# Optimization experiments

Hardware: AMD Instinct MI355X
Metric: run time of the kernel (lower is better)

Reference implementation:

```python
import jax, jax.numpy as jnp
import numpy as np

B, S, H, HS, BLK = 4, 4096, 16, 1024, 64
D = HS // H


def setup_inputs() -> dict:
    key = jax.random.key(0)
    ks = jax.random.split(key, 7)
    s = np.float32(1.0 / np.sqrt(HS))
    return {
        "hidden_states": jax.random.normal(ks[0], (B, S, HS), jnp.float32),
        "Wq": jax.random.normal(ks[1], (HS, HS), jnp.float32) * s,
        "bq": jax.random.normal(ks[2], (HS,), jnp.float32) * s,
        "Wk": jax.random.normal(ks[3], (HS, HS), jnp.float32) * s,
        "bk": jax.random.normal(ks[4], (HS,), jnp.float32) * s,
        "Wv": jax.random.normal(ks[5], (HS, HS), jnp.float32) * s,
        "bv": jax.random.normal(ks[6], (HS,), jnp.float32) * s,
    }


def reference(hidden_states, Wq, bq, Wk, bk, Wv, bv):
    b, m, _ = hidden_states.shape
    h, d, wm = H, D, BLK
    wn = wm
    nb = m // wm  # number of blocks
    scale = np.float32(1.0 / np.sqrt(d))

    def heads(x):  # [b, m, hs] -> [b, h, m, d]
        return x.reshape(b, m, h, d).transpose(0, 2, 1, 3)

    q = heads(hidden_states @ Wq.T + bq)
    k = heads(hidden_states @ Wk.T + bk)
    v = heads(hidden_states @ Wv.T + bv)

    qb = q.reshape(b, h, nb, wm, d)
    kb = k.reshape(b, h, nb, wn, d)
    vb = v.reshape(b, h, nb, wn, d)

    def attend(qx, kx, vx):  # qx [b,h,Q,d], kx/vx [b,h,K,d]
        scores = jnp.einsum('bhqd,bhkd->bhqk', qx, kx) * scale
        return jnp.einsum('bhqk,bhkd->bhqd', jax.nn.softmax(scores, axis=-1), vx)

    # first block: full attention over all keys
    first_ctx = attend(qb[:, :, 0], k, v)[:, :, None]

    # second block: keys = blocks [0, 1, 2, -1]
    k2 = jnp.concatenate([kb[:, :, 0], kb[:, :, 1], kb[:, :, 2], kb[:, :, -1]], axis=2)
    v2 = jnp.concatenate([vb[:, :, 0], vb[:, :, 1], vb[:, :, 2], vb[:, :, -1]], axis=2)
    second_ctx = attend(qb[:, :, 1], k2, v2)[:, :, None]

    # middle blocks 2..nb-3: sliding window of 3 key blocks + global first/last
    exp_k = jnp.concatenate([kb[:, :, 1:-3], kb[:, :, 2:-2], kb[:, :, 3:-1]], axis=3)  # [b,h,l,3wn,d]
    exp_v = jnp.concatenate([vb[:, :, 1:-3], vb[:, :, 2:-2], vb[:, :, 3:-1]], axis=3)
    mq = qb[:, :, 2:-2]  # [b,h,l,wm,d]
    inner = jnp.einsum('bhlqd,bhlkd->bhlqk', mq, exp_k) * scale
    first_band = jnp.einsum('bhlqd,bhkd->bhlqk', mq, kb[:, :, 0]) * scale
    last_band = jnp.einsum('bhlqd,bhkd->bhlqk', mq, kb[:, :, -1]) * scale
    band = jnp.concatenate([first_band, inner, last_band], axis=-1)  # [b,h,l,wm,5wn]
    aw = jax.nn.softmax(band, axis=-1)
    mid_ctx = jnp.einsum('bhlqk,bhlkd->bhlqd', aw[..., wn:4 * wn], exp_v)
    mid_ctx = mid_ctx + jnp.einsum('bhlqk,bhkd->bhlqd', aw[..., :wn], vb[:, :, 0])
    mid_ctx = mid_ctx + jnp.einsum('bhlqk,bhkd->bhlqd', aw[..., -wn:], vb[:, :, -1])

    # second-to-last block: keys = blocks [0, -3, -2, -1]
    k3 = jnp.concatenate([kb[:, :, 0], kb[:, :, -3], kb[:, :, -2], kb[:, :, -1]], axis=2)
    v3 = jnp.concatenate([vb[:, :, 0], vb[:, :, -3], vb[:, :, -2], vb[:, :, -1]], axis=2)
    second_last_ctx = attend(qb[:, :, -2], k3, v3)[:, :, None]

    # last block: full attention over all keys
    last_ctx = attend(qb[:, :, -1], k, v)[:, :, None]

    ctx = jnp.concatenate([first_ctx, second_ctx, mid_ctx, second_last_ctx, last_ctx], axis=2)
    return ctx.reshape(b, h, m, d).transpose(0, 2, 1, 3).reshape(b, m, h * d)
```

## Files before the change

kernel.cpp:

```cpp
#include <hip/hip_runtime.h>

typedef unsigned short u16;
using f32x4  = __attribute__((ext_vector_type(4))) float;
using bf16x8 = __attribute__((ext_vector_type(8))) short;

#define SEQ 4096
#define HS  1024
#define NHEAD 16
#define DH  64

__device__ __forceinline__ u16 f2bf(float f) {
  unsigned u = __float_as_uint(f);
  unsigned r = (u + 0x7fffu + ((u >> 16) & 1u)) >> 16;
  return (u16)r;
}

__device__ __forceinline__ void gl_lds16(const void* g, void* l) {
  __builtin_amdgcn_global_load_lds(
      (const __attribute__((address_space(1))) unsigned int*)g,
      (__attribute__((address_space(3))) unsigned int*)l, 16, 0, 0);
}

#define LGKM0 asm volatile("s_waitcnt lgkmcnt(0)" ::: "memory")
#define BARR  __builtin_amdgcn_s_barrier()

__global__ void cvt_all(const float* __restrict__ X, const float* __restrict__ Wq,
                        const float* __restrict__ Wk, const float* __restrict__ Wv,
                        u16* __restrict__ dst) {
  const int N = 19922944;
  int idx = blockIdx.x * blockDim.x + threadIdx.x;
  int stride = gridDim.x * blockDim.x;
  for (int i = idx * 4; i < N; i += stride * 4) {
    const float* s;
    if (i < 16777216)       s = X  + i;
    else if (i < 17825792)  s = Wq + (i - 16777216);
    else if (i < 18874368)  s = Wk + (i - 17825792);
    else                    s = Wv + (i - 18874368);
    float4 v = *reinterpret_cast<const float4*>(s);
    u16 o0 = f2bf(v.x), o1 = f2bf(v.y), o2 = f2bf(v.z), o3 = f2bf(v.w);
    unsigned lo = (unsigned)o0 | ((unsigned)o1 << 16);
    unsigned hi = (unsigned)o2 | ((unsigned)o3 << 16);
    uint2 pk; pk.x = lo; pk.y = hi;
    *reinterpret_cast<uint2*>(dst + i) = pk;
  }
}

__global__ __launch_bounds__(512) void gemm_qkv8(
    const u16* __restrict__ X,
    const u16* __restrict__ Wq, const u16* __restrict__ Wk, const u16* __restrict__ Wv,
    const float* __restrict__ bq, const float* __restrict__ bk, const float* __restrict__ bv,
    u16* __restrict__ Q, u16* __restrict__ K, u16* __restrict__ V) {
  __shared__ u16 lds[65536];

  const int tid = threadIdx.x;
  const int l = tid & 63;
  const int w = tid >> 6;
  const int wr = w >> 2;
  const int wc = w & 3;
  const int c = l & 15;
  const int g = l >> 4;

  int i = blockIdx.x;
  int k8 = i & 7, j8 = i >> 3;
  int w2 = j8 >> 5, r8 = j8 & 31;
  int np = w2 * 4 + (r8 >> 3);
  int mp = k8 * 8 + (r8 & 7);
  const int m0 = mp * 256;
  const int mat = np >> 2;
  const int n0 = (np & 3) * 256;
  const u16* W = (mat == 0) ? Wq : (mat == 1) ? Wk : Wv;
  const float* bias = (mat == 0) ? bq : (mat == 1) ? bk : bv;
  u16* O = (mat == 0) ? Q : (mat == 1) ? K : V;

  f32x4 acc[2][4][4] = {};

  auto stage = [&](const u16* G, int gbase, int ktile, int kh, int which) {
    u16* region = lds + ((ktile & 1) * 32768 + which * 16384 + kh * 8192);
#pragma unroll
    for (int ii = 0; ii < 2; ++ii) {
      int chunk = w * 2 + ii;
      int srow = chunk * 8 + (l >> 3);
      int slot = (l & 7) ^ (l >> 3);
      int grow = srow + ((slot >> 2) << 7);
      int ke = ktile * 64 + kh * 32 + (slot & 3) * 8;
      gl_lds16(G + (size_t)(gbase + grow) * HS + ke, region + chunk * 512);
    }
  };

  auto readA = [&](int cur, int CH, int KH, bf16x8* aq) {
    const char* base = (const char*)lds + cur * 65536 + KH * 16384;
    int colb = (wr * 64 + g * 16) ^ ((c & 7) << 4);
#pragma unroll
    for (int mf = 0; mf < 4; ++mf)
      aq[mf] = *reinterpret_cast<const bf16x8*>(base + (CH * 64 + mf * 16 + c) * 128 + colb);
  };
  auto readB = [&](int cur, int KH, bf16x8* bq2) {
    const char* base = (const char*)lds + cur * 65536 + 32768 + KH * 16384;
    int colb = ((wc >> 1) * 64 + g * 16) ^ ((c & 7) << 4);
#pragma unroll
    for (int nf = 0; nf < 4; ++nf)
      bq2[nf] = *reinterpret_cast<const bf16x8*>(base + ((wc & 1) * 64 + nf * 16 + c) * 128 + colb);
  };
  auto mma16 = [&](bf16x8* aq, bf16x8* bq2, f32x4 (*accr)[4]) {
    __builtin_amdgcn_s_setprio(1);
#pragma unroll
    for (int mf = 0; mf < 4; ++mf)
#pragma unroll
      for (int nf = 0; nf < 4; ++nf)
        accr[mf][nf] = __builtin_amdgcn_mfma_f32_16x16x32_bf16(aq[mf], bq2[nf], accr[mf][nf], 0, 0, 0);
    __builtin_amdgcn_s_setprio(0);
  };

  stage(X, m0, 0, 0, 0); stage(W, n0, 0, 0, 1);
  stage(X, m0, 0, 1, 0); stage(W, n0, 0, 1, 1);
  stage(X, m0, 1, 0, 0); stage(W, n0, 1, 0, 1);
  asm volatile("s_waitcnt vmcnt(4)" ::: "memory");
  BARR;

  for (int j = 0; j < 16; ++j) {
    const int cur = j & 1;
    bf16x8 aq[4], bq2[4];
    readA(cur, 0, 0, aq); readB(cur, 0, bq2);
    if (j + 1 < 16) stage(X, m0, j + 1, 1, 0);
    BARR; LGKM0; mma16(aq, bq2, acc[0]); BARR;
    readA(cur, 1, 0, aq);
    if (j + 1 < 16) stage(W, n0, j + 1, 1, 1);
    BARR; LGKM0; mma16(aq, bq2, acc[1]); BARR;
    readA(cur, 0, 1, aq); readB(cur, 1, bq2);
    if (j + 2 < 16) stage(X, m0, j + 2, 0, 0);
    BARR; LGKM0; mma16(aq, bq2, acc[0]); BARR;
    readA(cur, 1, 1, aq);
    if (j + 2 < 16) stage(W, n0, j + 2, 0, 1);
    BARR; LGKM0; mma16(aq, bq2, acc[1]);
    if (j < 14)       asm volatile("s_waitcnt vmcnt(4)" ::: "memory");
    else if (j == 14) asm volatile("s_waitcnt vmcnt(0)" ::: "memory");
    BARR;
  }

  __syncthreads();
  {
    u16* cst = lds;
#pragma unroll 1
    for (int p = 0; p < 2; ++p) {
      if (wr == p) {
#pragma unroll
        for (int nf = 0; nf < 4; ++nf) {
          int cc = wc * 64 + nf * 16 + c;
          float bval = bias[n0 + cc];
#pragma unroll
          for (int ch = 0; ch < 2; ++ch)
#pragma unroll
            for (int mf = 0; mf < 4; ++mf)
#pragma unroll
              for (int jj = 0; jj < 4; ++jj) {
                int rl = ch * 64 + mf * 16 + g * 4 + jj;
                cst[rl * 260 + cc] = f2bf(acc[ch][mf][nf][jj] + bval);
              }
        }
      }
      __syncthreads();
#pragma unroll
      for (int i2 = 0; i2 < 8; ++i2) {
        int row = i2 * 16 + (tid >> 5);
        int colu = (tid & 31) * 8;
        bf16x8 vv = *reinterpret_cast<const bf16x8*>(cst + row * 260 + colu);
        *reinterpret_cast<bf16x8*>(O + (size_t)(m0 + p * 128 + row) * HS + n0 + colu) = vv;
      }
      __syncthreads();
    }
  }
}

__global__ void bigbird_attn2(const u16* __restrict__ Q, const u16* __restrict__ K,
                              const u16* __restrict__ V, float* __restrict__ OUT,
                              float* __restrict__ Opart, float* __restrict__ MLpart) {
  __shared__ u16 Qs[64 * 64];
  __shared__ u16 Ks[2][64 * 64];
  __shared__ u16 Vt[64 * 72];
  __shared__ u16 Ps[64 * 72];

  const int tid = threadIdx.x;
  const int lane = tid & 63;
  const int w = tid >> 6;
  const int g = lane >> 4;
  const int c = lane & 15;

  int bid = blockIdx.x;
  int L = (bid & 7) * 624 + (bid >> 3);
  int g_bh = L / 78;
  int r = L - g_bh * 78;
  int b = g_bh & 3, h = g_bh >> 2;

  int qb, nkb, seg8 = 0, p = 0;
  bool heavy;
  if (r < 62) {
    heavy = false;
    qb = r + 1;
    nkb = (qb == 1 || qb == 62) ? 4 : 5;
  } else {
    heavy = true;
    int s = r - 62;
    int q2 = s >> 3, seg = s & 7;
    qb = q2 ? 63 : 0; seg8 = seg * 8; nkb = 8;
    p = ((q2 * 16 + h) * 4 + b) * 8 + seg;
  }

  const size_t base_bh = (size_t)b * SEQ * HS + (size_t)h * DH;

  auto kb_of = [&](int it) -> int {
    if (heavy) return seg8 + it;
    if (qb == 1)  return (it == 3) ? 63 : it;
    if (qb == 62) return (it == 0) ? 0 : 60 + it;
    return (it == 0) ? 0 : ((it == 4) ? 63 : qb - 2 + it);
  };

  const int vkrow = tid & 63;
  const int vdseg = (tid >> 6) * 16;

  {
    const u16* qg = Q + base_bh + (size_t)qb * 64 * HS;
#pragma unroll
    for (int t2 = 0; t2 < 2; ++t2) {
      int sub = w * 2 + t2;
      int rr = sub * 8 + (lane >> 3);
      int c16 = (lane & 7) ^ (rr & 7);
      gl_lds16(qg + (size_t)rr * HS + c16 * 8, Qs + sub * 512);
    }
  }
  int kb0 = kb_of(0);
  {
    const u16* kg = K + base_bh + (size_t)kb0 * 64 * HS;
#pragma unroll
    for (int t2 = 0; t2 < 2; ++t2) {
      int sub = w * 2 + t2;
      int rr = sub * 8 + (lane >> 3);
      int c16 = (lane & 7) ^ (rr & 7);
      gl_lds16(kg + (size_t)rr * HS + c16 * 8, Ks[0] + sub * 512);
    }
  }
  bf16x8 vr0, vr1;
  {
    const u16* vg = V + base_bh + (size_t)kb0 * 64 * HS;
    vr0 = *reinterpret_cast<const bf16x8*>(vg + (size_t)vkrow * HS + vdseg);
    vr1 = *reinterpret_cast<const bf16x8*>(vg + (size_t)vkrow * HS + vdseg + 8);
  }
  __syncthreads();

  bf16x8 qf[2];
#pragma unroll
  for (int ks = 0; ks < 2; ++ks) {
    int rr = w * 16 + c;
    int c16 = (ks * 4 + g) ^ (rr & 7);
    qf[ks] = *reinterpret_cast<const bf16x8*>(Qs + rr * 64 + c16 * 8);
  }

  float m_run = -1e30f, l_run = 0.f;
  f32x4 o_acc[4] = {};
  const float scale = 0.125f;

  for (int it = 0; it < nkb; ++it) {
    const int cur = it & 1;
    {
#pragma unroll
      for (int j2 = 0; j2 < 8; ++j2) {
        Vt[(vdseg + j2) * 72 + vkrow]     = (u16)vr0[j2];
        Vt[(vdseg + 8 + j2) * 72 + vkrow] = (u16)vr1[j2];
      }
    }
    if (it + 1 < nkb) {
      int kbn = kb_of(it + 1);
      const u16* kg = K + base_bh + (size_t)kbn * 64 * HS;
#pragma unroll
      for (int t2 = 0; t2 < 2; ++t2) {
        int sub = w * 2 + t2;
        int rr = sub * 8 + (lane >> 3);
        int c16 = (lane & 7) ^ (rr & 7);
        gl_lds16(kg + (size_t)rr * HS + c16 * 8, Ks[cur ^ 1] + sub * 512);
      }
      const u16* vg = V + base_bh + (size_t)kbn * 64 * HS;
      vr0 = *reinterpret_cast<const bf16x8*>(vg + (size_t)vkrow * HS + vdseg);
      vr1 = *reinterpret_cast<const bf16x8*>(vg + (size_t)vkrow * HS + vdseg + 8);
    }

    f32x4 accs[4] = {};
#pragma unroll
    for (int ks = 0; ks < 2; ++ks) {
#pragma unroll
      for (int mf = 0; mf < 4; ++mf) {
        int rr = mf * 16 + c;
        int c16 = (ks * 4 + g) ^ (rr & 7);
        bf16x8 kf = *reinterpret_cast<const bf16x8*>(Ks[cur] + rr * 64 + c16 * 8);
        accs[mf] = __builtin_amdgcn_mfma_f32_16x16x32_bf16(kf, qf[ks], accs[mf], 0, 0, 0);
      }
    }

    float sv[16];
    float smax = -1e30f;
#pragma unroll
    for (int mf = 0; mf < 4; ++mf)
#pragma unroll
      for (int j = 0; j < 4; ++j) {
        float s = accs[mf][j] * scale;
        sv[mf * 4 + j] = s;
        smax = fmaxf(smax, s);
      }
    smax = fmaxf(smax, __shfl_xor(smax, 16));
    smax = fmaxf(smax, __shfl_xor(smax, 32));
    float m_new = fmaxf(m_run, smax);
    float corr = __expf(m_run - m_new);
    float psum = 0.f;
    u16 pb[16];
#pragma unroll
    for (int i = 0; i < 16; ++i) {
      float pv = __expf(sv[i] - m_new);
      psum += pv;
      pb[i] = f2bf(pv);
    }
    psum += __shfl_xor(psum, 16);
    psum += __shfl_xor(psum, 32);
    l_run = l_run * corr + psum;
    m_run = m_new;

#pragma unroll
    for (int j = 0; j < 4; ++j) {
      float cj = __shfl(corr, g * 4 + j);
#pragma unroll
      for (int df = 0; df < 4; ++df) o_acc[df][j] *= cj;
    }

    {
      int rr = w * 16 + c;
#pragma unroll
      for (int mf = 0; mf < 4; ++mf) {
        unsigned lo = (unsigned)pb[mf * 4 + 0] | ((unsigned)pb[mf * 4 + 1] << 16);
        unsigned hi = (unsigned)pb[mf * 4 + 2] | ((unsigned)pb[mf * 4 + 3] << 16);
        uint2 pk; pk.x = lo; pk.y = hi;
        *reinterpret_cast<uint2*>(Ps + rr * 72 + mf * 16 + g * 4) = pk;
      }
    }

    __syncthreads();

#pragma unroll
    for (int ks = 0; ks < 2; ++ks) {
      bf16x8 pf = *reinterpret_cast<const bf16x8*>(Ps + (w * 16 + c) * 72 + ks * 32 + g * 8);
#pragma unroll
      for (int df = 0; df < 4; ++df) {
        bf16x8 vf = *reinterpret_cast<const bf16x8*>(Vt + (df * 16 + c) * 72 + ks * 32 + g * 8);
        o_acc[df] = __builtin_amdgcn_mfma_f32_16x16x32_bf16(pf, vf, o_acc[df], 0, 0, 0);
      }
    }

    __syncthreads();
  }

  if (!heavy) {
#pragma unroll
    for (int j = 0; j < 4; ++j) {
      float lr = __shfl(l_run, g * 4 + j);
      float inv = 1.f / lr;
      int rr = qb * 64 + w * 16 + g * 4 + j;
      size_t rowbase = ((size_t)b * SEQ + rr) * HS + (size_t)h * DH;
#pragma unroll
      for (int df = 0; df < 4; ++df)
        OUT[rowbase + df * 16 + c] = o_acc[df][j] * inv;
    }
  } else {
#pragma unroll
    for (int j = 0; j < 4; ++j) {
      int row = w * 16 + g * 4 + j;
#pragma unroll
      for (int df = 0; df < 4; ++df)
        Opart[(size_t)p * 4096 + row * 64 + df * 16 + c] = o_acc[df][j];
    }
    if (g == 0) {
      int row = w * 16 + c;
      MLpart[(size_t)p * 128 + row * 2]     = m_run;
      MLpart[(size_t)p * 128 + row * 2 + 1] = l_run;
    }
  }
}

__global__ void bigbird_combine(const float* __restrict__ Opart, const float* __restrict__ MLpart,
                                float* __restrict__ OUT) {
  int bid = blockIdx.x >> 2;
  int quarter = blockIdx.x & 3;
  int b = bid & 3; int t = bid >> 2; int h = t & 15; int q2 = t >> 4;
  int qb = q2 ? 63 : 0;
  int w = threadIdx.x >> 6, lane = threadIdx.x & 63;
  int pbase = ((q2 * 16 + h) * 4 + b) * 8;
#pragma unroll 1
  for (int j2 = 0; j2 < 4; ++j2) {
    int rr = quarter * 4 + j2;
    int row = w * 16 + rr;
    float ms[8], ls[8];
    float M = -1e30f;
#pragma unroll
    for (int s = 0; s < 8; ++s) {
      ms[s] = MLpart[(size_t)(pbase + s) * 128 + row * 2];
      ls[s] = MLpart[(size_t)(pbase + s) * 128 + row * 2 + 1];
      M = fmaxf(M, ms[s]);
    }
    float L = 0.f, acc = 0.f;
#pragma unroll
    for (int s = 0; s < 8; ++s) {
      float e = __expf(ms[s] - M);
      L += ls[s] * e;
      acc += e * Opart[(size_t)(pbase + s) * 4096 + row * 64 + lane];
    }
    int rq = qb * 64 + row;
    OUT[((size_t)b * SEQ + rq) * HS + (size_t)h * DH + lane] = acc / L;
  }
}

extern "C" void kernel_launch(void* const* d_in, const int* in_sizes, int n_in,
                              void* d_out, int out_size, void* d_ws, size_t ws_size,
                              hipStream_t stream) {
  const float* X  = (const float*)d_in[0];
  const float* Wq = (const float*)d_in[1];
  const float* bq = (const float*)d_in[2];
  const float* Wk = (const float*)d_in[3];
  const float* bk = (const float*)d_in[4];
  const float* Wv = (const float*)d_in[5];
  const float* bv = (const float*)d_in[6];
  float* out = (float*)d_out;

  u16* Xb  = (u16*)d_ws;
  u16* Wqb = Xb + 16777216;
  u16* Wkb = Wqb + 1048576;
  u16* Wvb = Wkb + 1048576;
  u16* Qb  = Wvb + 1048576;
  u16* Kb  = Qb + 16777216;
  u16* Vb  = Kb + 16777216;

  float* Opart  = (float*)Xb;
  float* MLpart = (float*)Wqb;

  cvt_all<<<2048, 256, 0, stream>>>(X, Wq, Wk, Wv, Xb);
  gemm_qkv8<<<768, 512, 0, stream>>>(Xb, Wqb, Wkb, Wvb, bq, bk, bv, Qb, Kb, Vb);
  bigbird_attn2<<<4992, 256, 0, stream>>>(Qb, Kb, Vb, out, Opart, MLpart);
  bigbird_combine<<<512, 256, 0, stream>>>(Opart, MLpart, out);
}
```

Measured before the change: 224.8 us.

## Pair adjacent query blocks per workgroup to share K/V tile loads

The attention kernel now handles two query blocks per 512-thread workgroup. It iterates over the union of their key blocks (6 for adjacent middle blocks) and masks out the key block that does not belong to each query half. This roughly halves K/V global loads and LDS staging per query block, and pairs the two heavy global rows with each other. In exchange, each workgroup does extra masked QK/softmax/PV work (6 iterations for two blocks versus 5 each) and runs half as many workgroups.

```diff
diff --git a/kernel.cpp b/kernel.cpp
--- a/kernel.cpp
+++ b/kernel.cpp
@@ -171,87 +171,78 @@
   }
 }
 
-__global__ void bigbird_attn2(const u16* __restrict__ Q, const u16* __restrict__ K,
-                              const u16* __restrict__ V, float* __restrict__ OUT,
-                              float* __restrict__ Opart, float* __restrict__ MLpart) {
-  __shared__ u16 Qs[64 * 64];
+__global__ __launch_bounds__(512) void bigbird_attn3(
+    const u16* __restrict__ Q, const u16* __restrict__ K,
+    const u16* __restrict__ V, float* __restrict__ OUT,
+    float* __restrict__ Opart, float* __restrict__ MLpart) {
+  __shared__ u16 Qs[2][64 * 64];
   __shared__ u16 Ks[2][64 * 64];
   __shared__ u16 Vt[64 * 72];
-  __shared__ u16 Ps[64 * 72];
+  __shared__ u16 Ps[128 * 72];
 
   const int tid = threadIdx.x;
   const int lane = tid & 63;
   const int w = tid >> 6;
+  const int w4 = w & 3;
+  const int qsel = w >> 2;
   const int g = lane >> 4;
   const int c = lane & 15;
 
   int bid = blockIdx.x;
-  int L = (bid & 7) * 624 + (bid >> 3);
-  int g_bh = L / 78;
-  int r = L - g_bh * 78;
+  int L = (bid & 7) * 312 + (bid >> 3);
+  int g_bh = L / 39;
+  int r = L - g_bh * 39;
   int b = g_bh & 3, h = g_bh >> 2;
 
-  int qb, nkb, seg8 = 0, p = 0;
-  bool heavy;
-  if (r < 62) {
-    heavy = false;
-    qb = r + 1;
-    nkb = (qb == 1 || qb == 62) ? 4 : 5;
-  } else {
-    heavy = true;
-    int s = r - 62;
-    int q2 = s >> 3, seg = s & 7;
-    qb = q2 ? 63 : 0; seg8 = seg * 8; nkb = 8;
-    p = ((q2 * 16 + h) * 4 + b) * 8 + seg;
-  }
+  int qbA, qbB, nkb, seg = 0;
+  bool heavy = false;
+  if (r < 30)       { qbA = 2 + 2 * r; qbB = qbA + 1; nkb = 6; }
+  else if (r == 30) { qbA = 1; qbB = 62; nkb = 6; }
+  else              { heavy = true; qbA = 0; qbB = 63; seg = r - 31; nkb = 8; }
 
   const size_t base_bh = (size_t)b * SEQ * HS + (size_t)h * DH;
+  const int myqb = qsel ? qbB : qbA;
 
   auto kb_of = [&](int it) -> int {
-    if (heavy) return seg8 + it;
-    if (qb == 1)  return (it == 3) ? 63 : it;
-    if (qb == 62) return (it == 0) ? 0 : 60 + it;
-    return (it == 0) ? 0 : ((it == 4) ? 63 : qb - 2 + it);
-  };
-
-  const int vkrow = tid & 63;
-  const int vdseg = (tid >> 6) * 16;
-
-  {
-    const u16* qg = Q + base_bh + (size_t)qb * 64 * HS;
-#pragma unroll
-    for (int t2 = 0; t2 < 2; ++t2) {
-      int sub = w * 2 + t2;
-      int rr = sub * 8 + (lane >> 3);
-      int c16 = (lane & 7) ^ (rr & 7);
-      gl_lds16(qg + (size_t)rr * HS + c16 * 8, Qs + sub * 512);
-    }
+    if (heavy) return seg * 8 + it;
+    if (r == 30) return (it < 3) ? it : 58 + it;
+    return (it == 0) ? 0 : ((it == 5) ? 63 : (qbA - 2 + it));
+  };
+  auto masked_of = [&](int it) -> bool {
+    if (heavy) return false;
+    if (r == 30) return qsel ? (it == 1 || it == 2) : (it == 3 || it == 4);
+    return qsel ? (it == 1) : (it == 4);
+  };
+
+#pragma unroll
+  for (int t2 = 0; t2 < 2; ++t2) {
+    const u16* qg = Q + base_bh + (size_t)(t2 ? qbB : qbA) * 64 * HS;
+    int rr = w * 8 + (lane >> 3);
+    int c16 = (lane & 7) ^ (rr & 7);
+    gl_lds16(qg + (size_t)rr * HS + c16 * 8, Qs[t2] + w * 512);
   }
   int kb0 = kb_of(0);
   {
     const u16* kg = K + base_bh + (size_t)kb0 * 64 * HS;
-#pragma unroll
-    for (int t2 = 0; t2 < 2; ++t2) {
-      int sub = w * 2 + t2;
-      int rr = sub * 8 + (lane >> 3);
-      int c16 = (lane & 7) ^ (rr & 7);
-      gl_lds16(kg + (size_t)rr * HS + c16 * 8, Ks[0] + sub * 512);
-    }
-  }
-  bf16x8 vr0, vr1;
+    int rr = w * 8 + (lane >> 3);
+    int c16 = (lane & 7) ^ (rr & 7);
+    gl_lds16(kg + (size_t)rr * HS + c16 * 8, Ks[0] + w * 512);
+  }
+  const int vkrow = lane;
+  const int vd8 = w * 8;
+  bf16x8 vr;
   {
     const u16* vg = V + base_bh + (size_t)kb0 * 64 * HS;
-    vr0 = *reinterpret_cast<const bf16x8*>(vg + (size_t)vkrow * HS + vdseg);
-    vr1 = *reinterpret_cast<const bf16x8*>(vg + (size_t)vkrow * HS + vdseg + 8);
+    vr = *reinterpret_cast<const bf16x8*>(vg + (size_t)vkrow * HS + vd8);
   }
   __syncthreads();
 
   bf16x8 qf[2];
 #pragma unroll
   for (int ks = 0; ks < 2; ++ks) {
-    int rr = w * 16 + c;
+    int rr = w4 * 16 + c;
     int c16 = (ks * 4 + g) ^ (rr & 7);
-    qf[ks] = *reinterpret_cast<const bf16x8*>(Qs + rr * 64 + c16 * 8);
+    qf[ks] = *reinterpret_cast<const bf16x8*>(Qs[qsel] + rr * 64 + c16 * 8);
   }
 
   float m_run = -1e30f, l_run = 0.f;
@@ -260,31 +251,22 @@
 
   for (int it = 0; it < nkb; ++it) {
     const int cur = it & 1;
-    {
-#pragma unroll
-      for (int j2 = 0; j2 < 8; ++j2) {
-        Vt[(vdseg + j2) * 72 + vkrow]     = (u16)vr0[j2];
-        Vt[(vdseg + 8 + j2) * 72 + vkrow] = (u16)vr1[j2];
-      }
-    }
+#pragma unroll
+    for (int j2 = 0; j2 < 8; ++j2)
+      Vt[(vd8 + j2) * 72 + vkrow] = (u16)vr[j2];
     if (it + 1 < nkb) {
       int kbn = kb_of(it + 1);
       const u16* kg = K + base_bh + (size_t)kbn * 64 * HS;
-#pragma unroll
-      for (int t2 = 0; t2 < 2; ++t2) {
-        int sub = w * 2 + t2;
-        int rr = sub * 8 + (lane >> 3);
-        int c16 = (lane & 7) ^ (rr & 7);
-        gl_lds16(kg + (size_t)rr * HS + c16 * 8, Ks[cur ^ 1] + sub * 512);
-      }
+      int rr = w * 8 + (lane >> 3);
+      int c16 = (lane & 7) ^ (rr & 7);
+      gl_lds16(kg + (size_t)rr * HS + c16 * 8, Ks[cur ^ 1] + w * 512);
       const u16* vg = V + base_bh + (size_t)kbn * 64 * HS;
-      vr0 = *reinterpret_cast<const bf16x8*>(vg + (size_t)vkrow * HS + vdseg);
-      vr1 = *reinterpret_cast<const bf16x8*>(vg + (size_t)vkrow * HS + vdseg + 8);
+      vr = *reinterpret_cast<const bf16x8*>(vg + (size_t)vkrow * HS + vd8);
     }
 
     f32x4 accs[4] = {};
 #pragma unroll
-    for (int ks = 0; ks < 2; ++ks) {
+    for (int ks = 0; ks < 2; ++ks)
 #pragma unroll
       for (int mf = 0; mf < 4; ++mf) {
         int rr = mf * 16 + c;
@@ -292,15 +274,15 @@
         bf16x8 kf = *reinterpret_cast<const bf16x8*>(Ks[cur] + rr * 64 + c16 * 8);
         accs[mf] = __builtin_amdgcn_mfma_f32_16x16x32_bf16(kf, qf[ks], accs[mf], 0, 0, 0);
       }
-    }
-
+
+    const bool msk = masked_of(it);
     float sv[16];
     float smax = -1e30f;
 #pragma unroll
     for (int mf = 0; mf < 4; ++mf)
 #pragma unroll
       for (int j = 0; j < 4; ++j) {
-        float s = accs[mf][j] * scale;
+        float s = msk ? -1e30f : accs[mf][j] * scale;
         sv[mf * 4 + j] = s;
         smax = fmaxf(smax, s);
       }
@@ -329,7 +311,7 @@
     }
 
     {
-      int rr = w * 16 + c;
+      int rr = qsel * 64 + w4 * 16 + c;
 #pragma unroll
       for (int mf = 0; mf < 4; ++mf) {
         unsigned lo = (unsigned)pb[mf * 4 + 0] | ((unsigned)pb[mf * 4 + 1] << 16);
@@ -343,7 +325,8 @@
 
 #pragma unroll
     for (int ks = 0; ks < 2; ++ks) {
-      bf16x8 pf = *reinterpret_cast<const bf16x8*>(Ps + (w * 16 + c) * 72 + ks * 32 + g * 8);
+      bf16x8 pf = *reinterpret_cast<const bf16x8*>(
+          Ps + (qsel * 64 + w4 * 16 + c) * 72 + ks * 32 + g * 8);
 #pragma unroll
       for (int df = 0; df < 4; ++df) {
         bf16x8 vf = *reinterpret_cast<const bf16x8*>(Vt + (df * 16 + c) * 72 + ks * 32 + g * 8);
@@ -359,22 +342,23 @@
     for (int j = 0; j < 4; ++j) {
       float lr = __shfl(l_run, g * 4 + j);
       float inv = 1.f / lr;
-      int rr = qb * 64 + w * 16 + g * 4 + j;
+      int rr = myqb * 64 + w4 * 16 + g * 4 + j;
       size_t rowbase = ((size_t)b * SEQ + rr) * HS + (size_t)h * DH;
 #pragma unroll
       for (int df = 0; df < 4; ++df)
         OUT[rowbase + df * 16 + c] = o_acc[df][j] * inv;
     }
   } else {
+    int p = ((qsel * 16 + h) * 4 + b) * 8 + seg;
 #pragma unroll
     for (int j = 0; j < 4; ++j) {
-      int row = w * 16 + g * 4 + j;
+      int row = w4 * 16 + g * 4 + j;
 #pragma unroll
       for (int df = 0; df < 4; ++df)
         Opart[(size_t)p * 4096 + row * 64 + df * 16 + c] = o_acc[df][j];
     }
     if (g == 0) {
-      int row = w * 16 + c;
+      int row = w4 * 16 + c;
       MLpart[(size_t)p * 128 + row * 2]     = m_run;
       MLpart[(size_t)p * 128 + row * 2 + 1] = l_run;
     }
@@ -438,6 +422,6 @@
 
   cvt_all<<<2048, 256, 0, stream>>>(X, Wq, Wk, Wv, Xb);
   gemm_qkv8<<<768, 512, 0, stream>>>(Xb, Wqb, Wkb, Wvb, bq, bk, bv, Qb, Kb, Vb);
-  bigbird_attn2<<<4992, 256, 0, stream>>>(Qb, Kb, Vb, out, Opart, MLpart);
+  bigbird_attn3<<<2496, 512, 0, stream>>>(Qb, Kb, Vb, out, Opart, MLpart);
   bigbird_combine<<<512, 256, 0, stream>>>(Opart, MLpart, out);
 }
```

Result: no change. 228.2 us (+1.5%).
